# Kernel tuning notes

Measured on AMD Instinct MI355X. Metric: run time of the kernel, lower is better.

The kernel has to match this reference:

```python
import jax, jax.numpy as jnp
import numpy as np

N_NODES = 100000
N_EDGES = 3200000
F_IN = 128
HIDDEN = 16
F_OUT = 2


def setup_inputs() -> dict:
    key = jax.random.key(0)
    k1, k2, k3, k4 = jax.random.split(key, 4)
    x = jax.random.normal(k1, (N_NODES, F_IN), dtype=jnp.float32)
    edge_index = jax.random.randint(k2, (2, N_EDGES), 0, N_NODES, dtype=jnp.int64)
    # Glorot-ish init like torch_geometric's GCNConv linear layers
    W1 = jax.random.normal(k3, (F_IN, HIDDEN), dtype=jnp.float32) * (1.0 / np.sqrt(F_IN))
    b1 = jnp.zeros((HIDDEN,), dtype=jnp.float32)
    W2 = jax.random.normal(k4, (HIDDEN, F_OUT), dtype=jnp.float32) * (1.0 / np.sqrt(HIDDEN))
    b2 = jnp.zeros((F_OUT,), dtype=jnp.float32)
    return {"x": x, "edge_index": edge_index, "W1": W1, "b1": b1, "W2": W2, "b2": b2}


def _gcn_conv(x, src, dst, W, b, num_nodes):
    """PyG GCNConv: out = D^{-1/2}(A+I)D^{-1/2} X W + b (self-loops included in src/dst)."""
    h = x @ W  # [N, F_out]
    ones = jnp.ones(src.shape[0], dtype=h.dtype)
    deg = jax.ops.segment_sum(ones, dst, num_segments=num_nodes)  # in-degree incl. self-loop
    deg_inv_sqrt = jnp.where(deg > 0, jax.lax.rsqrt(jnp.maximum(deg, 1.0)), 0.0)
    norm = deg_inv_sqrt[src] * deg_inv_sqrt[dst]  # [E+N]
    msg = h[src] * norm[:, None]  # gather + scale: [E+N, F_out]
    out = jax.ops.segment_sum(msg, dst, num_segments=num_nodes)  # scatter-add
    return out + b


def reference(x, edge_index, W1, b1, W2, b2):
    num_nodes = x.shape[0]
    self_loops = jnp.arange(num_nodes, dtype=edge_index.dtype)
    src = jnp.concatenate([edge_index[0], self_loops])
    dst = jnp.concatenate([edge_index[1], self_loops])
    h = jax.nn.relu(_gcn_conv(x, src, dst, W1, b1, num_nodes))
    # F.dropout(training=self.training) is identity in eval mode
    out = _gcn_conv(h, src, dst, W2, b2, num_nodes)
    return out
```

## Files before the change

kernel.cpp:

```cpp
#include <hip/hip_runtime.h>

#define N_NODES 100000
#define N_EDGES 3200000
#define F_IN    128
#define HIDDEN  16
#define F_OUT   2

#define BSZ     256
#define NB      391
#define NPAD    (NB * BSZ)
#define G       512
#define EPB     (N_EDGES / G)
#define DUMMY_E 100000u

typedef float  f32x4 __attribute__((ext_vector_type(4)));
typedef float  f32x2 __attribute__((ext_vector_type(2)));
typedef _Float16 half8 __attribute__((ext_vector_type(8)));
typedef _Float16 half4 __attribute__((ext_vector_type(4)));

__global__ __launch_bounds__(256) void k_hist(const int* __restrict__ dst,
                                              unsigned* __restrict__ blockHist) {
    __shared__ unsigned h0[NB];
    __shared__ unsigned h1[NB];
    int t = threadIdx.x, g = blockIdx.x;
    for (int i = t; i < NB; i += 256) { h0[i] = 0u; h1[i] = 0u; }
    __syncthreads();
    const int2* d2 = (const int2*)(dst + g * EPB);
    unsigned* myh = (t & 1) ? h1 : h0;
    for (int i = t; i < EPB / 2; i += 256) {
        int2 v = d2[i];
        atomicAdd(&myh[(unsigned)v.x >> 8], 1u);
        atomicAdd(&myh[(unsigned)v.y >> 8], 1u);
    }
    __syncthreads();
    for (int i = t; i < NB; i += 256) blockHist[i * G + g] = h0[i] + h1[i];
}

__global__ __launch_bounds__(G) void k_scan_blocks(unsigned* __restrict__ blockHist,
                                                   unsigned* __restrict__ total) {
    __shared__ unsigned s[G];
    int b = blockIdx.x, t = threadIdx.x;
    unsigned v = blockHist[b * G + t];
    s[t] = v;
    __syncthreads();
    for (int off = 1; off < G; off <<= 1) {
        unsigned xv = (t >= off) ? s[t - off] : 0u;
        __syncthreads();
        s[t] += xv;
        __syncthreads();
    }
    blockHist[b * G + t] = s[t] - v;
    if (t == G - 1) total[b] = s[t];
}

__global__ __launch_bounds__(512) void k_scan_buckets(const unsigned* __restrict__ total,
                                                      unsigned* __restrict__ bucketBase,
                                                      int* __restrict__ rowstart) {
    __shared__ unsigned s[512];
    int t = threadIdx.x;
    unsigned v = (t < NB) ? total[t] : 0u;
    s[t] = v;
    __syncthreads();
    for (int off = 1; off < 512; off <<= 1) {
        unsigned xv = (t >= off) ? s[t - off] : 0u;
        __syncthreads();
        s[t] += xv;
        __syncthreads();
    }
    if (t < NB) bucketBase[t] = s[t] - v;
    if (t == 511) {
        bucketBase[NB] = s[t];
        rowstart[N_NODES] = (int)s[t];
    }
}

__global__ __launch_bounds__(256) void k_scatter(const int* __restrict__ src,
                                                 const int* __restrict__ dst,
                                                 const unsigned* __restrict__ blockHist,
                                                 const unsigned* __restrict__ bucketBase,
                                                 unsigned* __restrict__ adj) {
    __shared__ unsigned stage[EPB];
    __shared__ unsigned short stage_b[EPB];
    __shared__ unsigned hist[NB];
    __shared__ unsigned h1[NB];
    __shared__ unsigned lstart[NB];
    __shared__ unsigned gbase[NB];
    __shared__ unsigned ssum[256];
    int t = threadIdx.x, g = blockIdx.x;
    for (int i = t; i < NB; i += 256) {
        hist[i] = 0u; h1[i] = 0u;
        gbase[i] = bucketBase[i] + blockHist[i * G + g];
    }
    __syncthreads();
    const int2* s2 = (const int2*)(src + g * EPB);
    const int2* d2 = (const int2*)(dst + g * EPB);
    unsigned* myh = (t & 1) ? h1 : hist;
    for (int i = t; i < EPB / 2; i += 256) {
        int2 v = d2[i];
        atomicAdd(&myh[(unsigned)v.x >> 8], 1u);
        atomicAdd(&myh[(unsigned)v.y >> 8], 1u);
    }
    __syncthreads();
    int i0 = t * 2;
    unsigned v0 = (i0 + 0 < NB) ? hist[i0 + 0] + h1[i0 + 0] : 0u;
    unsigned v1 = (i0 + 1 < NB) ? hist[i0 + 1] + h1[i0 + 1] : 0u;
    unsigned my = v0 + v1;
    ssum[t] = my;
    __syncthreads();
    for (int off = 1; off < 256; off <<= 1) {
        unsigned xv = (t >= off) ? ssum[t - off] : 0u;
        __syncthreads();
        ssum[t] += xv;
        __syncthreads();
    }
    unsigned e0 = ssum[t] - my;
    __syncthreads();
    unsigned e1 = e0 + v0;
    if (i0 + 0 < NB) { lstart[i0 + 0] = e0; hist[i0 + 0] = e0; }
    if (i0 + 1 < NB) { lstart[i0 + 1] = e1; hist[i0 + 1] = e1; }
    __syncthreads();
    for (int i = t; i < EPB / 2; i += 256) {
        int2 sv = s2[i], dv = d2[i];
        unsigned bkt0 = (unsigned)dv.x >> 8;
        unsigned pos0 = atomicAdd(&hist[bkt0], 1u);
        stage[pos0] = ((unsigned)(dv.x & 255) << 17) | (unsigned)sv.x;
        stage_b[pos0] = (unsigned short)bkt0;
        unsigned bkt1 = (unsigned)dv.y >> 8;
        unsigned pos1 = atomicAdd(&hist[bkt1], 1u);
        stage[pos1] = ((unsigned)(dv.y & 255) << 17) | (unsigned)sv.y;
        stage_b[pos1] = (unsigned short)bkt1;
    }
    __syncthreads();
    for (int j = t; j < EPB; j += 256) {
        unsigned bkt = stage_b[j];
        adj[gbase[bkt] + (j - lstart[bkt])] = stage[j];
    }
}

__global__ __launch_bounds__(256) void k_sortbucket(const unsigned* __restrict__ adj,
                                                    const unsigned* __restrict__ bucketBase,
                                                    unsigned* __restrict__ adj2,
                                                    int* __restrict__ rowstart,
                                                    float* __restrict__ dinv) {
    __shared__ unsigned hist[BSZ];
    __shared__ unsigned sc[BSZ];
    __shared__ unsigned cur[BSZ];
    int b = blockIdx.x, t = threadIdx.x;
    hist[t] = 0u;
    __syncthreads();
    int e0 = (int)bucketBase[b], e1 = (int)bucketBase[b + 1];
    for (int i = e0 + t; i < e1; i += 256) atomicAdd(&hist[adj[i] >> 17], 1u);
    __syncthreads();
    sc[t] = hist[t];
    __syncthreads();
    for (int off = 1; off < BSZ; off <<= 1) {
        unsigned a = (t >= off) ? sc[t - off] : 0u;
        __syncthreads();
        sc[t] += a;
        __syncthreads();
    }
    unsigned excl = sc[t] - hist[t];
    cur[t] = (unsigned)e0 + excl;
    int node = b * BSZ + t;
    if (node < N_NODES) {
        rowstart[node] = e0 + (int)excl;
        dinv[node] = rsqrtf((float)(hist[t] + 1u));
    }
    __syncthreads();
    for (int i = e0 + t; i < e1; i += 256) {
        unsigned v = adj[i];
        unsigned pos = atomicAdd(&cur[v >> 17], 1u);
        adj2[pos] = v & 0x1FFFFu;
    }
}

#define MM1_NODES 64
#define SXP 132
__global__ __launch_bounds__(256) void k_mm1(const float* __restrict__ x,
                                             const float* __restrict__ W1,
                                             const float* __restrict__ dinv,
                                             half4* __restrict__ hs) {
    __shared__ float sW[F_IN * HIDDEN];
    __shared__ float sX[MM1_NODES * SXP];
    int t = threadIdx.x;
    for (int i = t; i < F_IN * HIDDEN; i += 256) sW[i] = W1[i];
    int node0 = blockIdx.x * MM1_NODES;
    const float4* xv = (const float4*)(x + (size_t)node0 * F_IN);
    int maxv = (N_NODES - node0) * (F_IN / 4);
    if (maxv < 0) maxv = 0;
    for (int i = t; i < MM1_NODES * (F_IN / 4); i += 256) {
        if (i < maxv) {
            int nl = i >> 5, f4 = i & 31;
            ((float4*)(sX + nl * SXP))[f4] = xv[i];
        }
    }
    __syncthreads();
    int lane4 = t & 3;
    int nl = t >> 2;
    int n = node0 + nl;
    if (n >= NPAD) return;
    if (n >= N_NODES) {
        half4 hz = {(_Float16)0.f, (_Float16)0.f, (_Float16)0.f, (_Float16)0.f};
        hs[(size_t)n * 4 + lane4] = hz;
        return;
    }
    const float4* sWv = (const float4*)sW;
    float4 a = {0.f, 0.f, 0.f, 0.f};
    #pragma unroll 8
    for (int f = 0; f < F_IN; ++f) {
        float xval = sX[nl * SXP + f];
        float4 w = sWv[f * 4 + lane4];
        a.x = fmaf(xval, w.x, a.x);
        a.y = fmaf(xval, w.y, a.y);
        a.z = fmaf(xval, w.z, a.z);
        a.w = fmaf(xval, w.w, a.w);
    }
    float dv = dinv[n];
    half4 h; h[0] = (_Float16)(a.x * dv); h[1] = (_Float16)(a.y * dv);
    h[2] = (_Float16)(a.z * dv); h[3] = (_Float16)(a.w * dv);
    hs[(size_t)n * 4 + lane4] = h;
}

__global__ __launch_bounds__(256) void k_agg1(const unsigned* __restrict__ adj2,
                                              const int* __restrict__ rowstart,
                                              const char* __restrict__ hs,
                                              const float* __restrict__ dinv,
                                              const float* __restrict__ b1,
                                              const float* __restrict__ W2,
                                              float2* __restrict__ hs2) {
    int g = blockIdx.x * 256 + threadIdx.x;
    int node = g >> 1, le = g & 1;
    if (node >= N_NODES) {
        if (le == 0 && node < NPAD) { float2 z = {0.f, 0.f}; hs2[node] = z; }
        return;
    }
    int rs = rowstart[node], re = rowstart[node + 1];
    unsigned le16 = (unsigned)le * 16u;
    unsigned dummy_off = DUMMY_E * 32u + le16;

    float a0 = 0.f, a1 = 0.f, a2 = 0.f, a3 = 0.f, a4 = 0.f, a5 = 0.f, a6 = 0.f, a7 = 0.f;
    f32x4 w0, w1, w2, w3, w4, w5, w6, w7;

#define GL1(dst, o) asm volatile("global_load_dwordx4 %0, %1, %2" \
    : "=v"(dst) : "v"(o), "s"(hs) : "memory");
#define AC1(w_) { half8 h8; __builtin_memcpy(&h8, &w_, 16); \
    a0 += (float)h8[0]; a1 += (float)h8[1]; a2 += (float)h8[2]; a3 += (float)h8[3]; \
    a4 += (float)h8[4]; a5 += (float)h8[5]; a6 += (float)h8[6]; a7 += (float)h8[7]; }

    for (int bs = rs; bs < re; bs += 8) {
        const unsigned* ap = adj2 + bs;
        unsigned j0 = ap[0], j1 = ap[1], j2 = ap[2], j3 = ap[3];
        unsigned j4 = ap[4], j5 = ap[5], j6 = ap[6], j7 = ap[7];
        unsigned o0 = (bs + 0 < re) ? (j0 << 5) + le16 : dummy_off;
        unsigned o1 = (bs + 1 < re) ? (j1 << 5) + le16 : dummy_off;
        unsigned o2 = (bs + 2 < re) ? (j2 << 5) + le16 : dummy_off;
        unsigned o3 = (bs + 3 < re) ? (j3 << 5) + le16 : dummy_off;
        unsigned o4 = (bs + 4 < re) ? (j4 << 5) + le16 : dummy_off;
        unsigned o5 = (bs + 5 < re) ? (j5 << 5) + le16 : dummy_off;
        unsigned o6 = (bs + 6 < re) ? (j6 << 5) + le16 : dummy_off;
        unsigned o7 = (bs + 7 < re) ? (j7 << 5) + le16 : dummy_off;
        GL1(w0, o0) GL1(w1, o1) GL1(w2, o2) GL1(w3, o3)
        GL1(w4, o4) GL1(w5, o5) GL1(w6, o6) GL1(w7, o7)
        asm volatile("s_waitcnt vmcnt(0)" ::: "memory");
        __builtin_amdgcn_sched_barrier(0);
        AC1(w0) AC1(w1) AC1(w2) AC1(w3) AC1(w4) AC1(w5) AC1(w6) AC1(w7)
    }
    const _Float16* selfrow = (const _Float16*)(hs + (size_t)node * 32 + le16);
    float dv = dinv[node];
    float q0 = dv * (a0 + (float)selfrow[0]), q1 = dv * (a1 + (float)selfrow[1]);
    float q2 = dv * (a2 + (float)selfrow[2]), q3 = dv * (a3 + (float)selfrow[3]);
    float q4 = dv * (a4 + (float)selfrow[4]), q5 = dv * (a5 + (float)selfrow[5]);
    float q6 = dv * (a6 + (float)selfrow[6]), q7 = dv * (a7 + (float)selfrow[7]);
    const float4* b1v = (const float4*)(b1 + le * 8);
    float4 ba = b1v[0], bb = b1v[1];
    const float4* w2v = (const float4*)(W2 + le * 16);
    float4 wA = w2v[0], wB = w2v[1], wC = w2v[2], wD = w2v[3];
    float p0 = 0.f, p1 = 0.f, r;
    r = fmaxf(q0 + ba.x, 0.f); p0 = fmaf(r, wA.x, p0); p1 = fmaf(r, wA.y, p1);
    r = fmaxf(q1 + ba.y, 0.f); p0 = fmaf(r, wA.z, p0); p1 = fmaf(r, wA.w, p1);
    r = fmaxf(q2 + ba.z, 0.f); p0 = fmaf(r, wB.x, p0); p1 = fmaf(r, wB.y, p1);
    r = fmaxf(q3 + ba.w, 0.f); p0 = fmaf(r, wB.z, p0); p1 = fmaf(r, wB.w, p1);
    r = fmaxf(q4 + bb.x, 0.f); p0 = fmaf(r, wC.x, p0); p1 = fmaf(r, wC.y, p1);
    r = fmaxf(q5 + bb.y, 0.f); p0 = fmaf(r, wC.z, p0); p1 = fmaf(r, wC.w, p1);
    r = fmaxf(q6 + bb.z, 0.f); p0 = fmaf(r, wD.x, p0); p1 = fmaf(r, wD.y, p1);
    r = fmaxf(q7 + bb.w, 0.f); p0 = fmaf(r, wD.z, p0); p1 = fmaf(r, wD.w, p1);
    p0 += __shfl_xor(p0, 1);
    p1 += __shfl_xor(p1, 1);
    if (le == 0) {
        float2 h2; h2.x = p0 * dv; h2.y = p1 * dv;
        hs2[node] = h2;
    }
}

__global__ __launch_bounds__(256) void k_agg2(const unsigned* __restrict__ adj2,
                                              const int* __restrict__ rowstart,
                                              const char* __restrict__ hs2,
                                              const float* __restrict__ dinv,
                                              const float* __restrict__ b2,
                                              float2* __restrict__ out) {
    int node = blockIdx.x * 256 + threadIdx.x;
    if (node >= N_NODES) return;
    int rs = rowstart[node], re = rowstart[node + 1];
    unsigned dummy_off = DUMMY_E * 8u;

    float a0 = 0.f, a1 = 0.f;
    f32x2 w0, w1, w2, w3, w4, w5, w6, w7;

#define GL2(dst, o) asm volatile("global_load_dwordx2 %0, %1, %2" \
    : "=v"(dst) : "v"(o), "s"(hs2) : "memory");

    for (int bs = rs; bs < re; bs += 8) {
        const unsigned* ap = adj2 + bs;
        unsigned j0 = ap[0], j1 = ap[1], j2 = ap[2], j3 = ap[3];
        unsigned j4 = ap[4], j5 = ap[5], j6 = ap[6], j7 = ap[7];
        unsigned o0 = (bs + 0 < re) ? (j0 << 3) : dummy_off;
        unsigned o1 = (bs + 1 < re) ? (j1 << 3) : dummy_off;
        unsigned o2 = (bs + 2 < re) ? (j2 << 3) : dummy_off;
        unsigned o3 = (bs + 3 < re) ? (j3 << 3) : dummy_off;
        unsigned o4 = (bs + 4 < re) ? (j4 << 3) : dummy_off;
        unsigned o5 = (bs + 5 < re) ? (j5 << 3) : dummy_off;
        unsigned o6 = (bs + 6 < re) ? (j6 << 3) : dummy_off;
        unsigned o7 = (bs + 7 < re) ? (j7 << 3) : dummy_off;
        GL2(w0, o0) GL2(w1, o1) GL2(w2, o2) GL2(w3, o3)
        GL2(w4, o4) GL2(w5, o5) GL2(w6, o6) GL2(w7, o7)
        asm volatile("s_waitcnt vmcnt(0)" ::: "memory");
        __builtin_amdgcn_sched_barrier(0);
        a0 += w0[0] + w1[0] + w2[0] + w3[0] + w4[0] + w5[0] + w6[0] + w7[0];
        a1 += w0[1] + w1[1] + w2[1] + w3[1] + w4[1] + w5[1] + w6[1] + w7[1];
    }
    const float2* h2p = (const float2*)hs2;
    float2 selfv = h2p[node];
    float dv = dinv[node];
    float2 r;
    r.x = fmaf(dv, a0 + selfv.x, b2[0]);
    r.y = fmaf(dv, a1 + selfv.y, b2[1]);
    out[node] = r;
}

extern "C" void kernel_launch(void* const* d_in, const int* in_sizes, int n_in,
                              void* d_out, int out_size, void* d_ws, size_t ws_size,
                              hipStream_t stream) {
    const float* x   = (const float*)d_in[0];
    const int*   ei  = (const int*)d_in[1];
    const int*   srcv = ei;
    const int*   dstv = ei + N_EDGES;
    const float* W1  = (const float*)d_in[2];
    const float* b1  = (const float*)d_in[3];
    const float* W2  = (const float*)d_in[4];
    const float* b2  = (const float*)d_in[5];
    float* out = (float*)d_out;

    char* w = (char*)d_ws;
    unsigned* adj        = (unsigned*)w;  w += (size_t)N_EDGES * 4;
    unsigned* adj2       = (unsigned*)w;  w += (size_t)(N_EDGES + 8) * 4;
    unsigned* blockHist  = (unsigned*)w;  w += (size_t)NB * G * 4;
    unsigned* total      = (unsigned*)w;  w += (size_t)NB * 4;
    unsigned* bucketBase = (unsigned*)w;  w += (size_t)(NB + 1) * 4;
    int*      rowstart   = (int*)w;       w += (size_t)(N_NODES + 1) * 4;
    w = (char*)(((size_t)w + 15) & ~(size_t)15);
    float* dinv  = (float*)w;  w += (size_t)N_NODES * 4;
    char*  hs    = w;          w += (size_t)NPAD * HIDDEN * 2;
    float* hs2   = (float*)w;

    k_hist        <<<G, 256, 0, stream>>>(dstv, blockHist);
    k_scan_blocks <<<NB, G, 0, stream>>>(blockHist, total);
    k_scan_buckets<<<1, 512, 0, stream>>>(total, bucketBase, rowstart);
    k_scatter     <<<G, 256, 0, stream>>>(srcv, dstv, blockHist, bucketBase, adj);
    k_sortbucket  <<<NB, 256, 0, stream>>>(adj, bucketBase, adj2, rowstart, dinv);
    k_mm1         <<<NPAD / MM1_NODES, 256, 0, stream>>>(x, W1, dinv, (half4*)hs);
    k_agg1        <<<(2 * NPAD) / 256, 256, 0, stream>>>(adj2, rowstart, hs, dinv,
                                                         b1, W2, (float2*)hs2);
    k_agg2        <<<(NPAD + 255) / 256, 256, 0, stream>>>(adj2, rowstart, (const char*)hs2,
                                                           dinv, b2, (float2*)out);
}
```

Before: 126.8 us.

## Replace global histogram scans with fixed-capacity buckets and atomic cursors

Removes the separate histogram, block-scan and bucket-scan kernels. Each bucket now gets a fixed-capacity region (CAP slots), and every scatter block claims its offset within that region through a global atomicAdd on a per-bucket cursor. Row start and end are stored as separate arrays, and hs/hs2 reuse the adj buffer once it is no longer needed. This cuts three kernel launches and one full pass over dst, at the cost of assuming no bucket exceeds CAP edges and of a non-deterministic edge order within each bucket.

```diff
diff --git a/kernel.cpp b/kernel.cpp
--- a/kernel.cpp
+++ b/kernel.cpp
@@ -11,6 +11,7 @@
 #define NPAD    (NB * BSZ)
 #define G       512
 #define EPB     (N_EDGES / G)
+#define CAP     9216
 #define DUMMY_E 100000u
 
 typedef float  f32x4 __attribute__((ext_vector_type(4)));
@@ -18,13 +19,26 @@
 typedef _Float16 half8 __attribute__((ext_vector_type(8)));
 typedef _Float16 half4 __attribute__((ext_vector_type(4)));
 
-__global__ __launch_bounds__(256) void k_hist(const int* __restrict__ dst,
-                                              unsigned* __restrict__ blockHist) {
+__global__ __launch_bounds__(512) void k_init(unsigned* __restrict__ cursor) {
+    int t = threadIdx.x;
+    if (t < NB) cursor[t] = 0u;
+}
+
+__global__ __launch_bounds__(256) void k_scatter(const int* __restrict__ src,
+                                                 const int* __restrict__ dst,
+                                                 unsigned* __restrict__ cursor,
+                                                 unsigned* __restrict__ adj) {
+    __shared__ unsigned stage[EPB];
+    __shared__ unsigned short stage_b[EPB];
     __shared__ unsigned h0[NB];
     __shared__ unsigned h1[NB];
+    __shared__ unsigned lstart[NB];
+    __shared__ unsigned gbase[NB];
+    __shared__ unsigned ssum[256];
     int t = threadIdx.x, g = blockIdx.x;
     for (int i = t; i < NB; i += 256) { h0[i] = 0u; h1[i] = 0u; }
     __syncthreads();
+    const int2* s2 = (const int2*)(src + g * EPB);
     const int2* d2 = (const int2*)(dst + g * EPB);
     unsigned* myh = (t & 1) ? h1 : h0;
     for (int i = t; i < EPB / 2; i += 256) {
@@ -33,77 +47,9 @@
         atomicAdd(&myh[(unsigned)v.y >> 8], 1u);
     }
     __syncthreads();
-    for (int i = t; i < NB; i += 256) blockHist[i * G + g] = h0[i] + h1[i];
-}
-
-__global__ __launch_bounds__(G) void k_scan_blocks(unsigned* __restrict__ blockHist,
-                                                   unsigned* __restrict__ total) {
-    __shared__ unsigned s[G];
-    int b = blockIdx.x, t = threadIdx.x;
-    unsigned v = blockHist[b * G + t];
-    s[t] = v;
-    __syncthreads();
-    for (int off = 1; off < G; off <<= 1) {
-        unsigned xv = (t >= off) ? s[t - off] : 0u;
-        __syncthreads();
-        s[t] += xv;
-        __syncthreads();
-    }
-    blockHist[b * G + t] = s[t] - v;
-    if (t == G - 1) total[b] = s[t];
-}
-
-__global__ __launch_bounds__(512) void k_scan_buckets(const unsigned* __restrict__ total,
-                                                      unsigned* __restrict__ bucketBase,
-                                                      int* __restrict__ rowstart) {
-    __shared__ unsigned s[512];
-    int t = threadIdx.x;
-    unsigned v = (t < NB) ? total[t] : 0u;
-    s[t] = v;
-    __syncthreads();
-    for (int off = 1; off < 512; off <<= 1) {
-        unsigned xv = (t >= off) ? s[t - off] : 0u;
-        __syncthreads();
-        s[t] += xv;
-        __syncthreads();
-    }
-    if (t < NB) bucketBase[t] = s[t] - v;
-    if (t == 511) {
-        bucketBase[NB] = s[t];
-        rowstart[N_NODES] = (int)s[t];
-    }
-}
-
-__global__ __launch_bounds__(256) void k_scatter(const int* __restrict__ src,
-                                                 const int* __restrict__ dst,
-                                                 const unsigned* __restrict__ blockHist,
-                                                 const unsigned* __restrict__ bucketBase,
-                                                 unsigned* __restrict__ adj) {
-    __shared__ unsigned stage[EPB];
-    __shared__ unsigned short stage_b[EPB];
-    __shared__ unsigned hist[NB];
-    __shared__ unsigned h1[NB];
-    __shared__ unsigned lstart[NB];
-    __shared__ unsigned gbase[NB];
-    __shared__ unsigned ssum[256];
-    int t = threadIdx.x, g = blockIdx.x;
-    for (int i = t; i < NB; i += 256) {
-        hist[i] = 0u; h1[i] = 0u;
-        gbase[i] = bucketBase[i] + blockHist[i * G + g];
-    }
-    __syncthreads();
-    const int2* s2 = (const int2*)(src + g * EPB);
-    const int2* d2 = (const int2*)(dst + g * EPB);
-    unsigned* myh = (t & 1) ? h1 : hist;
-    for (int i = t; i < EPB / 2; i += 256) {
-        int2 v = d2[i];
-        atomicAdd(&myh[(unsigned)v.x >> 8], 1u);
-        atomicAdd(&myh[(unsigned)v.y >> 8], 1u);
-    }
-    __syncthreads();
     int i0 = t * 2;
-    unsigned v0 = (i0 + 0 < NB) ? hist[i0 + 0] + h1[i0 + 0] : 0u;
-    unsigned v1 = (i0 + 1 < NB) ? hist[i0 + 1] + h1[i0 + 1] : 0u;
+    unsigned v0 = (i0 + 0 < NB) ? h0[i0 + 0] + h1[i0 + 0] : 0u;
+    unsigned v1 = (i0 + 1 < NB) ? h0[i0 + 1] + h1[i0 + 1] : 0u;
     unsigned my = v0 + v1;
     ssum[t] = my;
     __syncthreads();
@@ -116,31 +62,38 @@
     unsigned e0 = ssum[t] - my;
     __syncthreads();
     unsigned e1 = e0 + v0;
-    if (i0 + 0 < NB) { lstart[i0 + 0] = e0; hist[i0 + 0] = e0; }
-    if (i0 + 1 < NB) { lstart[i0 + 1] = e1; hist[i0 + 1] = e1; }
+    if (i0 + 0 < NB) {
+        lstart[i0 + 0] = e0; h0[i0 + 0] = e0;
+        gbase[i0 + 0] = atomicAdd(&cursor[i0 + 0], v0);
+    }
+    if (i0 + 1 < NB) {
+        lstart[i0 + 1] = e1; h0[i0 + 1] = e1;
+        gbase[i0 + 1] = atomicAdd(&cursor[i0 + 1], v1);
+    }
     __syncthreads();
     for (int i = t; i < EPB / 2; i += 256) {
         int2 sv = s2[i], dv = d2[i];
-        unsigned bkt0 = (unsigned)dv.x >> 8;
-        unsigned pos0 = atomicAdd(&hist[bkt0], 1u);
-        stage[pos0] = ((unsigned)(dv.x & 255) << 17) | (unsigned)sv.x;
-        stage_b[pos0] = (unsigned short)bkt0;
-        unsigned bkt1 = (unsigned)dv.y >> 8;
-        unsigned pos1 = atomicAdd(&hist[bkt1], 1u);
-        stage[pos1] = ((unsigned)(dv.y & 255) << 17) | (unsigned)sv.y;
-        stage_b[pos1] = (unsigned short)bkt1;
+        unsigned b0 = (unsigned)dv.x >> 8;
+        unsigned p0 = atomicAdd(&h0[b0], 1u);
+        stage[p0] = ((unsigned)(dv.x & 255) << 17) | (unsigned)sv.x;
+        stage_b[p0] = (unsigned short)b0;
+        unsigned b1 = (unsigned)dv.y >> 8;
+        unsigned p1 = atomicAdd(&h0[b1], 1u);
+        stage[p1] = ((unsigned)(dv.y & 255) << 17) | (unsigned)sv.y;
+        stage_b[p1] = (unsigned short)b1;
     }
     __syncthreads();
     for (int j = t; j < EPB; j += 256) {
         unsigned bkt = stage_b[j];
-        adj[gbase[bkt] + (j - lstart[bkt])] = stage[j];
+        adj[(unsigned)bkt * CAP + gbase[bkt] + (j - lstart[bkt])] = stage[j];
     }
 }
 
 __global__ __launch_bounds__(256) void k_sortbucket(const unsigned* __restrict__ adj,
-                                                    const unsigned* __restrict__ bucketBase,
+                                                    const unsigned* __restrict__ cursor,
                                                     unsigned* __restrict__ adj2,
-                                                    int* __restrict__ rowstart,
+                                                    int* __restrict__ rsA,
+                                                    int* __restrict__ reA,
                                                     float* __restrict__ dinv) {
     __shared__ unsigned hist[BSZ];
     __shared__ unsigned sc[BSZ];
@@ -148,7 +101,7 @@
     int b = blockIdx.x, t = threadIdx.x;
     hist[t] = 0u;
     __syncthreads();
-    int e0 = (int)bucketBase[b], e1 = (int)bucketBase[b + 1];
+    int e0 = b * CAP, e1 = e0 + (int)cursor[b];
     for (int i = e0 + t; i < e1; i += 256) atomicAdd(&hist[adj[i] >> 17], 1u);
     __syncthreads();
     sc[t] = hist[t];
@@ -163,7 +116,8 @@
     cur[t] = (unsigned)e0 + excl;
     int node = b * BSZ + t;
     if (node < N_NODES) {
-        rowstart[node] = e0 + (int)excl;
+        rsA[node] = e0 + (int)excl;
+        reA[node] = e0 + (int)(excl + hist[t]);
         dinv[node] = rsqrtf((float)(hist[t] + 1u));
     }
     __syncthreads();
@@ -222,7 +176,8 @@
 }
 
 __global__ __launch_bounds__(256) void k_agg1(const unsigned* __restrict__ adj2,
-                                              const int* __restrict__ rowstart,
+                                              const int* __restrict__ rsA,
+                                              const int* __restrict__ reA,
                                               const char* __restrict__ hs,
                                               const float* __restrict__ dinv,
                                               const float* __restrict__ b1,
@@ -234,7 +189,7 @@
         if (le == 0 && node < NPAD) { float2 z = {0.f, 0.f}; hs2[node] = z; }
         return;
     }
-    int rs = rowstart[node], re = rowstart[node + 1];
+    int rs0 = rsA[node], re0 = reA[node];
     unsigned le16 = (unsigned)le * 16u;
     unsigned dummy_off = DUMMY_E * 32u + le16;
 
@@ -247,18 +202,18 @@
     a0 += (float)h8[0]; a1 += (float)h8[1]; a2 += (float)h8[2]; a3 += (float)h8[3]; \
     a4 += (float)h8[4]; a5 += (float)h8[5]; a6 += (float)h8[6]; a7 += (float)h8[7]; }
 
-    for (int bs = rs; bs < re; bs += 8) {
+    for (int bs = rs0; bs < re0; bs += 8) {
         const unsigned* ap = adj2 + bs;
         unsigned j0 = ap[0], j1 = ap[1], j2 = ap[2], j3 = ap[3];
         unsigned j4 = ap[4], j5 = ap[5], j6 = ap[6], j7 = ap[7];
-        unsigned o0 = (bs + 0 < re) ? (j0 << 5) + le16 : dummy_off;
-        unsigned o1 = (bs + 1 < re) ? (j1 << 5) + le16 : dummy_off;
-        unsigned o2 = (bs + 2 < re) ? (j2 << 5) + le16 : dummy_off;
-        unsigned o3 = (bs + 3 < re) ? (j3 << 5) + le16 : dummy_off;
-        unsigned o4 = (bs + 4 < re) ? (j4 << 5) + le16 : dummy_off;
-        unsigned o5 = (bs + 5 < re) ? (j5 << 5) + le16 : dummy_off;
-        unsigned o6 = (bs + 6 < re) ? (j6 << 5) + le16 : dummy_off;
-        unsigned o7 = (bs + 7 < re) ? (j7 << 5) + le16 : dummy_off;
+        unsigned o0 = (bs + 0 < re0) ? (j0 << 5) + le16 : dummy_off;
+        unsigned o1 = (bs + 1 < re0) ? (j1 << 5) + le16 : dummy_off;
+        unsigned o2 = (bs + 2 < re0) ? (j2 << 5) + le16 : dummy_off;
+        unsigned o3 = (bs + 3 < re0) ? (j3 << 5) + le16 : dummy_off;
+        unsigned o4 = (bs + 4 < re0) ? (j4 << 5) + le16 : dummy_off;
+        unsigned o5 = (bs + 5 < re0) ? (j5 << 5) + le16 : dummy_off;
+        unsigned o6 = (bs + 6 < re0) ? (j6 << 5) + le16 : dummy_off;
+        unsigned o7 = (bs + 7 < re0) ? (j7 << 5) + le16 : dummy_off;
         GL1(w0, o0) GL1(w1, o1) GL1(w2, o2) GL1(w3, o3)
         GL1(w4, o4) GL1(w5, o5) GL1(w6, o6) GL1(w7, o7)
         asm volatile("s_waitcnt vmcnt(0)" ::: "memory");
@@ -293,14 +248,15 @@
 }
 
 __global__ __launch_bounds__(256) void k_agg2(const unsigned* __restrict__ adj2,
-                                              const int* __restrict__ rowstart,
+                                              const int* __restrict__ rsA,
+                                              const int* __restrict__ reA,
                                               const char* __restrict__ hs2,
                                               const float* __restrict__ dinv,
                                               const float* __restrict__ b2,
                                               float2* __restrict__ out) {
     int node = blockIdx.x * 256 + threadIdx.x;
     if (node >= N_NODES) return;
-    int rs = rowstart[node], re = rowstart[node + 1];
+    int rs0 = rsA[node], re0 = reA[node];
     unsigned dummy_off = DUMMY_E * 8u;
 
     float a0 = 0.f, a1 = 0.f;
@@ -309,18 +265,18 @@
 #define GL2(dst, o) asm volatile("global_load_dwordx2 %0, %1, %2" \
     : "=v"(dst) : "v"(o), "s"(hs2) : "memory");
 
-    for (int bs = rs; bs < re; bs += 8) {
+    for (int bs = rs0; bs < re0; bs += 8) {
         const unsigned* ap = adj2 + bs;
         unsigned j0 = ap[0], j1 = ap[1], j2 = ap[2], j3 = ap[3];
         unsigned j4 = ap[4], j5 = ap[5], j6 = ap[6], j7 = ap[7];
-        unsigned o0 = (bs + 0 < re) ? (j0 << 3) : dummy_off;
-        unsigned o1 = (bs + 1 < re) ? (j1 << 3) : dummy_off;
-        unsigned o2 = (bs + 2 < re) ? (j2 << 3) : dummy_off;
-        unsigned o3 = (bs + 3 < re) ? (j3 << 3) : dummy_off;
-        unsigned o4 = (bs + 4 < re) ? (j4 << 3) : dummy_off;
-        unsigned o5 = (bs + 5 < re) ? (j5 << 3) : dummy_off;
-        unsigned o6 = (bs + 6 < re) ? (j6 << 3) : dummy_off;
-        unsigned o7 = (bs + 7 < re) ? (j7 << 3) : dummy_off;
+        unsigned o0 = (bs + 0 < re0) ? (j0 << 3) : dummy_off;
+        unsigned o1 = (bs + 1 < re0) ? (j1 << 3) : dummy_off;
+        unsigned o2 = (bs + 2 < re0) ? (j2 << 3) : dummy_off;
+        unsigned o3 = (bs + 3 < re0) ? (j3 << 3) : dummy_off;
+        unsigned o4 = (bs + 4 < re0) ? (j4 << 3) : dummy_off;
+        unsigned o5 = (bs + 5 < re0) ? (j5 << 3) : dummy_off;
+        unsigned o6 = (bs + 6 < re0) ? (j6 << 3) : dummy_off;
+        unsigned o7 = (bs + 7 < re0) ? (j7 << 3) : dummy_off;
         GL2(w0, o0) GL2(w1, o1) GL2(w2, o2) GL2(w3, o3)
         GL2(w4, o4) GL2(w5, o5) GL2(w6, o6) GL2(w7, o7)
         asm volatile("s_waitcnt vmcnt(0)" ::: "memory");
@@ -351,25 +307,21 @@
     float* out = (float*)d_out;
 
     char* w = (char*)d_ws;
-    unsigned* adj        = (unsigned*)w;  w += (size_t)N_EDGES * 4;
-    unsigned* adj2       = (unsigned*)w;  w += (size_t)(N_EDGES + 8) * 4;
-    unsigned* blockHist  = (unsigned*)w;  w += (size_t)NB * G * 4;
-    unsigned* total      = (unsigned*)w;  w += (size_t)NB * 4;
-    unsigned* bucketBase = (unsigned*)w;  w += (size_t)(NB + 1) * 4;
-    int*      rowstart   = (int*)w;       w += (size_t)(N_NODES + 1) * 4;
-    w = (char*)(((size_t)w + 15) & ~(size_t)15);
-    float* dinv  = (float*)w;  w += (size_t)N_NODES * 4;
-    char*  hs    = w;          w += (size_t)NPAD * HIDDEN * 2;
-    float* hs2   = (float*)w;
-
-    k_hist        <<<G, 256, 0, stream>>>(dstv, blockHist);
-    k_scan_blocks <<<NB, G, 0, stream>>>(blockHist, total);
-    k_scan_buckets<<<1, 512, 0, stream>>>(total, bucketBase, rowstart);
-    k_scatter     <<<G, 256, 0, stream>>>(srcv, dstv, blockHist, bucketBase, adj);
-    k_sortbucket  <<<NB, 256, 0, stream>>>(adj, bucketBase, adj2, rowstart, dinv);
-    k_mm1         <<<NPAD / MM1_NODES, 256, 0, stream>>>(x, W1, dinv, (half4*)hs);
-    k_agg1        <<<(2 * NPAD) / 256, 256, 0, stream>>>(adj2, rowstart, hs, dinv,
-                                                         b1, W2, (float2*)hs2);
-    k_agg2        <<<(NPAD + 255) / 256, 256, 0, stream>>>(adj2, rowstart, (const char*)hs2,
-                                                           dinv, b2, (float2*)out);
-}
+    unsigned* adj    = (unsigned*)w;  w += (size_t)NB * CAP * 4;
+    unsigned* adj2   = (unsigned*)w;  w += (size_t)(NB * CAP + 8) * 4;
+    unsigned* cursor = (unsigned*)w;  w += (size_t)NB * 4;
+    int*      rsA    = (int*)w;       w += (size_t)N_NODES * 4;
+    int*      reA    = (int*)w;       w += (size_t)N_NODES * 4;
+    float*    dinv   = (float*)w;     w += (size_t)N_NODES * 4;
+    char*  hs  = (char*)adj;
+    float* hs2 = (float*)(hs + (size_t)NPAD * HIDDEN * 2);
+
+    k_init       <<<1, 512, 0, stream>>>(cursor);
+    k_scatter    <<<G, 256, 0, stream>>>(srcv, dstv, cursor, adj);
+    k_sortbucket <<<NB, 256, 0, stream>>>(adj, cursor, adj2, rsA, reA, dinv);
+    k_mm1        <<<NPAD / MM1_NODES, 256, 0, stream>>>(x, W1, dinv, (half4*)hs);
+    k_agg1       <<<(2 * NPAD) / 256, 256, 0, stream>>>(adj2, rsA, reA, hs, dinv,
+                                                        b1, W2, (float2*)hs2);
+    k_agg2       <<<(NPAD + 255) / 256, 256, 0, stream>>>(adj2, rsA, reA, (const char*)hs2,
+                                                          dinv, b2, (float2*)out);
+}
```

New measurement: 146.5 us. 1.16x slower.
